# Performance work log

Measured on AMD Instinct MI355X. Metric: run time of the kernel, lower is better.

Reference implementation:

```python
import jax, jax.numpy as jnp
import numpy as np

EMBED_DIM = 32
DELTA_V = 0.5
DELTA_D = 3.0
NUM_LABELS = 20  # instance labels are 1..NUM_LABELS; 0 is background


def _safe_sqrt(x):
    # sqrt with zero-safe gradient (matches norm of identical points -> 0)
    s = jnp.where(x > 0, x, 1.0)
    return jnp.where(x > 0, jnp.sqrt(s), 0.0)


def _per_batch(emb, seg):
    # emb: [D, N], seg: [N] int labels in 0..L (0 = background)
    D, N = emb.shape
    L = NUM_LABELS
    dt = emb.dtype
    ones = jnp.ones((N,), dt)
    counts = jax.ops.segment_sum(ones, seg, num_segments=L + 1)          # [L+1]
    sums = jax.ops.segment_sum(emb.T, seg, num_segments=L + 1)          # [L+1, D]
    means = sums / jnp.maximum(counts, 1.0)[:, None]                     # [L+1, D]
    present = (counts > 0).at[0].set(False)                              # [L+1]
    num_lanes = jnp.sum(present.astype(dt))

    # --- variance (pull) loss: each pixel vs its own instance centroid ---
    mpix = means[seg]                                                    # [N, D] gather
    sq = jnp.sum((emb.T - mpix) ** 2, axis=1)                            # [N]
    d = _safe_sqrt(sq)
    v = jnp.maximum(d - DELTA_V, 0.0) ** 2 * (seg > 0).astype(dt)        # background excluded
    vsum = jax.ops.segment_sum(v, seg, num_segments=L + 1)               # [L+1]
    vmean = vsum / jnp.maximum(counts, 1.0)
    var_loss = jnp.sum(vmean * present.astype(dt)) / jnp.maximum(num_lanes, 1.0)
    var_loss = jnp.where(num_lanes > 0, var_loss, jnp.zeros((), dt))

    # --- distance (push) loss between present centroids ---
    m = means[1:]                                                        # [L, D]
    p = present[1:]                                                      # [L]
    sqd = jnp.sum((m[:, None, :] - m[None, :, :]) ** 2, axis=-1)         # [L, L]
    dist = _safe_sqrt(sqd)
    pair = (p[:, None] & p[None, :]) & ~jnp.eye(L, dtype=bool)
    dl = jnp.sum(jnp.maximum(DELTA_D - dist, 0.0) ** 2 * pair.astype(dt))
    denom = jnp.maximum(num_lanes * (num_lanes - 1.0), 1.0)
    dist_loss = jnp.where(num_lanes > 1, dl / denom / 2.0, jnp.zeros((), dt))
    return var_loss, dist_loss


def setup_inputs() -> dict:
    key = jax.random.key(0)
    k1, k2 = jax.random.split(key)
    B, D, N = 8, EMBED_DIM, 65536  # 256x256 BEV raster flattened
    embedding = jax.random.normal(k1, (B, D, N), dtype=jnp.float32)
    seg_gt = jax.random.randint(k2, (B, N), 0, NUM_LABELS + 1, dtype=jnp.int32)
    return {"embedding": embedding, "seg_gt": seg_gt}


def reference(embedding, seg_gt):
    var_b, dist_b = jax.vmap(_per_batch)(embedding, seg_gt)  # [B], [B]
    var_loss = jnp.mean(var_b)
    dist_loss = jnp.mean(dist_b)
    reg_loss = jnp.zeros((), embedding.dtype)
    return (var_loss, dist_loss, reg_loss)
```

## Files before the change

### kernel.cpp

```cpp
#include <hip/hip_runtime.h>
#include <hip/hip_cooperative_groups.h>
namespace cg = cooperative_groups;

#define NSEG 21
#define NLBL 20
#define DIM  32
#define NS   64
#define NREP 16
#define DV   0.5f
#define DD   3.0f
#define BATCH 8
#define N_PIX 65536
#define SMS  36
#define DYNB (128*512 + 1024)

using short8 = __attribute__((ext_vector_type(8))) short;
using f32x4  = __attribute__((ext_vector_type(4))) float;

#define P_OFF  0
#define C2_OFF (BATCH*DIM*NLBL*NS)
#define M_OFF  (C2_OFF + BATCH*NLBL*NS)
#define CN_OFF (M_OFF + BATCH*NLBL*DIM)
#define V_OFF  (CN_OFF + BATCH*NLBL)
#define PB_OFF (V_OFF + BATCH*NLBL*NS)

__device__ __forceinline__ short bf16rne(float f) {
  const unsigned u = __builtin_bit_cast(unsigned, f);
  return (short)((u + 0x7FFFu + ((u >> 16) & 1u)) >> 16);
}

__device__ __forceinline__ void momentsBody(const float* __restrict__ emb,
                                            const int* __restrict__ seg,
                                            float* __restrict__ ws,
                                            float* lred, ushort* tile,
                                            unsigned char* segt,
                                            int bx, int b, int tid) {
  const int wv = tid >> 6, lane = tid & 63;
  const int lr = lane & 15, lg = lane >> 4;
  const float* rowA0 = emb + ((size_t)b * DIM + lr) * N_PIX;
  const float* rowA1 = rowA0 + (size_t)16 * N_PIX;
  const int*   segb  = seg + (size_t)b * N_PIX;

  f32x4 s00 = {0,0,0,0}, s01 = {0,0,0,0}, s10 = {0,0,0,0}, s11 = {0,0,0,0};
  f32x4 c0  = {0,0,0,0}, c1  = {0,0,0,0};
  short8 ones;
  #pragma unroll
  for (int j = 0; j < 8; ++j) ones[j] = (short)0x3F80;

  #pragma unroll 2
  for (int t = 0; t < 8; ++t) {
    const int kl = wv * 256 + t * 32 + lg * 8;
    const int koff = bx * 1024 + kl;
    const float4 a00 = *(const float4*)(rowA0 + koff);
    const float4 a01 = *(const float4*)(rowA0 + koff + 4);
    const float4 a10 = *(const float4*)(rowA1 + koff);
    const float4 a11 = *(const float4*)(rowA1 + koff + 4);
    const int4   g0  = *(const int4*)(segb + koff);
    const int4   g1  = *(const int4*)(segb + koff + 4);

    short8 fa0, fa1, fb0, fb1;
    fa0[0] = bf16rne(a00.x); fa0[1] = bf16rne(a00.y);
    fa0[2] = bf16rne(a00.z); fa0[3] = bf16rne(a00.w);
    fa0[4] = bf16rne(a01.x); fa0[5] = bf16rne(a01.y);
    fa0[6] = bf16rne(a01.z); fa0[7] = bf16rne(a01.w);
    fa1[0] = bf16rne(a10.x); fa1[1] = bf16rne(a10.y);
    fa1[2] = bf16rne(a10.z); fa1[3] = bf16rne(a10.w);
    fa1[4] = bf16rne(a11.x); fa1[5] = bf16rne(a11.y);
    fa1[6] = bf16rne(a11.z); fa1[7] = bf16rne(a11.w);
    const int lab0 = lr + 1, lab1 = lr + 17;
    fb0[0] = (g0.x == lab0) ? (short)0x3F80 : (short)0;
    fb0[1] = (g0.y == lab0) ? (short)0x3F80 : (short)0;
    fb0[2] = (g0.z == lab0) ? (short)0x3F80 : (short)0;
    fb0[3] = (g0.w == lab0) ? (short)0x3F80 : (short)0;
    fb0[4] = (g1.x == lab0) ? (short)0x3F80 : (short)0;
    fb0[5] = (g1.y == lab0) ? (short)0x3F80 : (short)0;
    fb0[6] = (g1.z == lab0) ? (short)0x3F80 : (short)0;
    fb0[7] = (g1.w == lab0) ? (short)0x3F80 : (short)0;
    fb1[0] = (g0.x == lab1) ? (short)0x3F80 : (short)0;
    fb1[1] = (g0.y == lab1) ? (short)0x3F80 : (short)0;
    fb1[2] = (g0.z == lab1) ? (short)0x3F80 : (short)0;
    fb1[3] = (g0.w == lab1) ? (short)0x3F80 : (short)0;
    fb1[4] = (g1.x == lab1) ? (short)0x3F80 : (short)0;
    fb1[5] = (g1.y == lab1) ? (short)0x3F80 : (short)0;
    fb1[6] = (g1.z == lab1) ? (short)0x3F80 : (short)0;
    fb1[7] = (g1.w == lab1) ? (short)0x3F80 : (short)0;

    const int o = kl >> 3, om = o & 7;
    *(short8*)&tile[o * 256 + ((lr ^ om) << 3)] = fa0;
    *(short8*)&tile[o * 256 + (((lr ^ om) + 16) << 3)] = fa1;
    if (lr == 0) {
      unsigned long long pk =
          (unsigned long long)(g0.x & 255)        | ((unsigned long long)(g0.y & 255) << 8) |
          ((unsigned long long)(g0.z & 255) << 16) | ((unsigned long long)(g0.w & 255) << 24) |
          ((unsigned long long)(g1.x & 255) << 32) | ((unsigned long long)(g1.y & 255) << 40) |
          ((unsigned long long)(g1.z & 255) << 48) | ((unsigned long long)(g1.w & 255) << 56);
      *(unsigned long long*)&segt[o * 8] = pk;
    }

    s00 = __builtin_amdgcn_mfma_f32_16x16x32_bf16(fa0, fb0, s00, 0, 0, 0);
    s01 = __builtin_amdgcn_mfma_f32_16x16x32_bf16(fa0, fb1, s01, 0, 0, 0);
    s10 = __builtin_amdgcn_mfma_f32_16x16x32_bf16(fa1, fb0, s10, 0, 0, 0);
    s11 = __builtin_amdgcn_mfma_f32_16x16x32_bf16(fa1, fb1, s11, 0, 0, 0);
    c0  = __builtin_amdgcn_mfma_f32_16x16x32_bf16(ones, fb0, c0, 0, 0, 0);
    c1  = __builtin_amdgcn_mfma_f32_16x16x32_bf16(ones, fb1, c1, 0, 0, 0);
  }

  float vals[24];
  #pragma unroll
  for (int r = 0; r < 4; ++r) {
    vals[0 * 4 + r] = s00[r]; vals[1 * 4 + r] = s01[r];
    vals[2 * 4 + r] = s10[r]; vals[3 * 4 + r] = s11[r];
    vals[4 * 4 + r] = c0[r];  vals[5 * 4 + r] = c1[r];
  }
  #pragma unroll
  for (int w = 0; w < 4; ++w) {
    if (wv == w) {
      float* base = lred + lane * 4;
      if (w == 0) {
        #pragma unroll
        for (int f = 0; f < 6; ++f)
          #pragma unroll
          for (int r = 0; r < 4; ++r) base[f * 256 + r] = vals[f * 4 + r];
      } else {
        #pragma unroll
        for (int f = 0; f < 6; ++f)
          #pragma unroll
          for (int r = 0; r < 4; ++r) base[f * 256 + r] += vals[f * 4 + r];
      }
    }
    __syncthreads();
  }
  for (int i = tid; i < 1536; i += 256) {
    const float v = lred[i];
    const int f = i >> 8, ln = (i >> 2) & 63, r = i & 3;
    const int col = ln & 15, row = ((ln >> 4) << 2) | r;
    if (f < 4) {
      const int d = (f >> 1) * 16 + row;
      const int lcol = (f & 1) * 16 + col;
      if (lcol < NLBL)
        ws[P_OFF + (((size_t)(b * DIM + d) * NLBL) + lcol) * NS + bx] = v;
    } else {
      const int lcol = (f & 1) * 16 + col;
      if (row == 0 && lcol < NLBL)
        ws[C2_OFF + ((size_t)b * NLBL + lcol) * NS + bx] = v;
    }
  }
}

__device__ __forceinline__ void meansBody(float* __restrict__ ws, float* s_c,
                                          int bx8, int b, int tid) {
  if (tid < NLBL) {
    const float4* cp = (const float4*)(ws + C2_OFF + ((size_t)b * NLBL + tid) * NS);
    float q0 = 0.f, q1 = 0.f, q2 = 0.f, q3 = 0.f;
    #pragma unroll
    for (int k = 0; k < NS / 4; k += 4) {
      const float4 v0 = cp[k], v1 = cp[k + 1], v2 = cp[k + 2], v3 = cp[k + 3];
      q0 += v0.x + v0.y + v0.z + v0.w;
      q1 += v1.x + v1.y + v1.z + v1.w;
      q2 += v2.x + v2.y + v2.z + v2.w;
      q3 += v3.x + v3.y + v3.z + v3.w;
    }
    const float c = q0 + q1 + q2 + q3;
    if (bx8 == 0) ws[CN_OFF + b * NLBL + tid] = c;
    s_c[tid] = fmaxf(c, 1.f);
  }
  __syncthreads();
  if (tid < 80) {
    const int m = bx8 * 80 + tid;
    const int l = m >> 5, d = m & 31;
    const float4* pp = (const float4*)(ws + P_OFF + (((size_t)(b * DIM + d) * NLBL) + l) * NS);
    float q0 = 0.f, q1 = 0.f, q2 = 0.f, q3 = 0.f;
    #pragma unroll
    for (int k = 0; k < NS / 4; k += 4) {
      const float4 v0 = pp[k], v1 = pp[k + 1], v2 = pp[k + 2], v3 = pp[k + 3];
      q0 += v0.x + v0.y + v0.z + v0.w;
      q1 += v1.x + v1.y + v1.z + v1.w;
      q2 += v2.x + v2.y + v2.z + v2.w;
      q3 += v3.x + v3.y + v3.z + v3.w;
    }
    ws[M_OFF + (size_t)b * NLBL * DIM + m] = (q0 + q1 + q2 + q3) / s_c[l];
  }
}

__device__ __forceinline__ void loadMeans(const float* __restrict__ ws,
                                          float* s_m, int b, int tid) {
  for (int i = tid; i < NSEG * SMS; i += 256) s_m[i] = 0.f;
  __syncthreads();
  if (tid < 160) {
    const float4 v = ((const float4*)(ws + M_OFF + (size_t)b * NLBL * DIM))[tid];
    const int flat = tid * 4, l = flat >> 5, d = flat & 31;
    float* dst = &s_m[(l + 1) * SMS + d];
    dst[0] = v.x; dst[1] = v.y; dst[2] = v.z; dst[3] = v.w;
  }
}

__device__ __forceinline__ void finalBody(float* __restrict__ ws,
                                          float* s_m, float* s_c, float* s_vs,
                                          int* s_p, float* s_red, int b, int tid) {
  const int wv = tid >> 6, lane = tid & 63;
  if (tid < 160) {
    const int g = tid >> 3, j = tid & 7;
    const float4* v4 = (const float4*)(ws + V_OFF + ((size_t)b * NLBL + g) * NS + j * 8);
    const float4 a = v4[0], c = v4[1];
    float s = a.x + a.y + a.z + a.w + c.x + c.y + c.z + c.w;
    s += __shfl_xor(s, 1, 64); s += __shfl_xor(s, 2, 64); s += __shfl_xor(s, 4, 64);
    if (j == 0) s_vs[g] = s;
  }
  if (tid < NLBL) {
    const float c = ws[CN_OFF + b * NLBL + tid];
    s_c[tid] = c;
    s_p[tid] = (c > 0.f) ? 1 : 0;
  }
  __syncthreads();
  loadMeans(ws, s_m, b, tid);
  __syncthreads();

  float dl = 0.f;
  for (int p = tid; p < NLBL * NLBL; p += 256) {
    const int i = p / NLBL, j = p - (p / NLBL) * NLBL;
    if (i != j && s_p[i] && s_p[j]) {
      float sq = 0.f;
      #pragma unroll
      for (int d = 0; d < DIM; ++d) {
        const float t = s_m[(i + 1) * SMS + d] - s_m[(j + 1) * SMS + d];
        sq += t * t;
      }
      const float r = DD - sqrtf(sq);
      if (r > 0.f) dl += r * r;
    }
  }
  #pragma unroll
  for (int off = 32; off; off >>= 1) dl += __shfl_xor(dl, off, 64);
  if (lane == 0) s_red[wv] = dl;
  __syncthreads();
  if (tid == 0) {
    const float dsum = s_red[0] + s_red[1] + s_red[2] + s_red[3];
    float nl = 0.f, var = 0.f;
    for (int l = 0; l < NLBL; ++l)
      if (s_p[l]) { nl += 1.f; var += s_vs[l] / s_c[l]; }
    ws[PB_OFF + b * 2]     = (nl > 0.f) ? var / nl : 0.f;
    ws[PB_OFF + b * 2 + 1] = (nl > 1.f) ? dsum / fmaxf(nl * (nl - 1.f), 1.f) * 0.5f : 0.f;
  }
}

__device__ __forceinline__ void outBody(const float* __restrict__ ws,
                                        float* __restrict__ out, int tid) {
  if (tid < 64) {
    float v = 0.f, d = 0.f;
    if (tid < BATCH) {
      v = ws[PB_OFF + tid * 2];
      d = ws[PB_OFF + tid * 2 + 1];
    }
    #pragma unroll
    for (int off = 4; off; off >>= 1) { v += __shfl_xor(v, off, 64); d += __shfl_xor(d, off, 64); }
    if (tid == 0) {
      out[0] = v / (float)BATCH;
      out[1] = d / (float)BATCH;
      out[2] = 0.f;
    }
  }
}

__global__ __launch_bounds__(256, 2)
void k_fused(const float* __restrict__ emb, const int* __restrict__ seg,
             float* __restrict__ ws, float* __restrict__ out) {
  extern __shared__ __align__(16) char dynls[];
  ushort* tile = (ushort*)dynls;
  unsigned char* segt = (unsigned char*)(dynls + 65536);
  __shared__ __align__(16) float lred[1536];
  __shared__ __align__(16) float s_m[NSEG * SMS];
  __shared__ float s_v[NREP * NSEG];
  __shared__ float s_c[NLBL];
  __shared__ float s_vs[NLBL];
  __shared__ int   s_p[NLBL];
  __shared__ float s_red[4];
  cg::grid_group gg = cg::this_grid();
  const int tid = threadIdx.x, bx = blockIdx.x, b = blockIdx.y;

  momentsBody(emb, seg, ws, lred, tile, segt, bx, b, tid);
  gg.sync();
  if (bx < 8) meansBody(ws, s_c, bx, b, tid);
  gg.sync();

  for (int i = tid; i < NREP * NSEG; i += 256) s_v[i] = 0.f;
  loadMeans(ws, s_m, b, tid);
  __syncthreads();
  {
    const int px0 = tid * 4;
    const int o = px0 >> 3, om = o & 7, p8 = px0 & 7;
    const int la0 = segt[px0], la1 = segt[px0 + 1], la2 = segt[px0 + 2], la3 = segt[px0 + 3];
    float q0 = 0.f, q1 = 0.f, q2 = 0.f, q3 = 0.f;
    #pragma unroll
    for (int db = 0; db < 8; ++db) {
      const f32x4 m0 = *(const f32x4*)&s_m[la0 * SMS + db * 4];
      const f32x4 m1 = *(const f32x4*)&s_m[la1 * SMS + db * 4];
      const f32x4 m2 = *(const f32x4*)&s_m[la2 * SMS + db * 4];
      const f32x4 m3 = *(const f32x4*)&s_m[la3 * SMS + db * 4];
      #pragma unroll
      for (int dd = 0; dd < 4; ++dd) {
        const int d = db * 4 + dd;
        const ushort4 ev = *(const ushort4*)&tile[o * 256 + ((d ^ om) << 3) + p8];
        float t;
        t = __builtin_bit_cast(float, (unsigned)ev.x << 16) - m0[dd]; q0 += t * t;
        t = __builtin_bit_cast(float, (unsigned)ev.y << 16) - m1[dd]; q1 += t * t;
        t = __builtin_bit_cast(float, (unsigned)ev.z << 16) - m2[dd]; q2 += t * t;
        t = __builtin_bit_cast(float, (unsigned)ev.w << 16) - m3[dd]; q3 += t * t;
      }
    }
    const int rb = (tid & (NREP - 1)) * NSEG;
    if (la0 > 0) { const float r = sqrtf(q0) - DV; if (r > 0.f) atomicAdd(&s_v[rb + la0], r * r); }
    if (la1 > 0) { const float r = sqrtf(q1) - DV; if (r > 0.f) atomicAdd(&s_v[rb + la1], r * r); }
    if (la2 > 0) { const float r = sqrtf(q2) - DV; if (r > 0.f) atomicAdd(&s_v[rb + la2], r * r); }
    if (la3 > 0) { const float r = sqrtf(q3) - DV; if (r > 0.f) atomicAdd(&s_v[rb + la3], r * r); }
  }
  __syncthreads();
  if (tid < NLBL) {
    float v = 0.f;
    #pragma unroll
    for (int r = 0; r < NREP; ++r) v += s_v[r * NSEG + (tid + 1)];
    ws[V_OFF + ((size_t)b * NLBL + tid) * NS + bx] = v;
  }
  gg.sync();
  if (bx == 0) finalBody(ws, s_m, s_c, s_vs, s_p, s_red, b, tid);
  gg.sync();
  if (bx == 0 && b == 0) outBody(ws, out, tid);
}

__global__ __launch_bounds__(256)
void k_moments(const float* __restrict__ emb, const int* __restrict__ seg,
               float* __restrict__ ws) {
  extern __shared__ __align__(16) char dynls[];
  ushort* tile = (ushort*)dynls;
  unsigned char* segt = (unsigned char*)(dynls + 65536);
  __shared__ __align__(16) float lred[1536];
  momentsBody(emb, seg, ws, lred, tile, segt, blockIdx.x, blockIdx.y, threadIdx.x);
}
__global__ __launch_bounds__(256)
void k_means(float* __restrict__ ws) {
  __shared__ float s_c[NLBL];
  meansBody(ws, s_c, blockIdx.x, blockIdx.y, threadIdx.x);
}
__global__ __launch_bounds__(256)
void k_varG(const float* __restrict__ emb, const int* __restrict__ seg,
            float* __restrict__ ws) {
  __shared__ __align__(16) float s_m[NSEG * SMS];
  __shared__ float s_v[NREP * NSEG];
  const int tid = threadIdx.x, bx = blockIdx.x, b = blockIdx.y;
  for (int i = tid; i < NREP * NSEG; i += 256) s_v[i] = 0.f;
  loadMeans(ws, s_m, b, tid);
  __syncthreads();
  const int n0 = bx * 1024 + tid * 4;
  const int4 sl = *(const int4*)(seg + (size_t)b * N_PIX + n0);
  const float4* e4 = (const float4*)(emb + (size_t)b * DIM * N_PIX + n0);
  float q0 = 0.f, q1 = 0.f, q2 = 0.f, q3 = 0.f;
  #pragma unroll 8
  for (int d = 0; d < DIM; ++d) {
    const float4 e = e4[d * (N_PIX / 4)];
    float t;
    t = e.x - s_m[sl.x * SMS + d]; q0 += t * t;
    t = e.y - s_m[sl.y * SMS + d]; q1 += t * t;
    t = e.z - s_m[sl.z * SMS + d]; q2 += t * t;
    t = e.w - s_m[sl.w * SMS + d]; q3 += t * t;
  }
  const int rb = (tid & (NREP - 1)) * NSEG;
  if (sl.x > 0) { const float r = sqrtf(q0) - DV; if (r > 0.f) atomicAdd(&s_v[rb + sl.x], r * r); }
  if (sl.y > 0) { const float r = sqrtf(q1) - DV; if (r > 0.f) atomicAdd(&s_v[rb + sl.y], r * r); }
  if (sl.z > 0) { const float r = sqrtf(q2) - DV; if (r > 0.f) atomicAdd(&s_v[rb + sl.z], r * r); }
  if (sl.w > 0) { const float r = sqrtf(q3) - DV; if (r > 0.f) atomicAdd(&s_v[rb + sl.w], r * r); }
  __syncthreads();
  if (tid < NLBL) {
    float v = 0.f;
    #pragma unroll
    for (int r = 0; r < NREP; ++r) v += s_v[r * NSEG + (tid + 1)];
    ws[V_OFF + ((size_t)b * NLBL + tid) * NS + bx] = v;
  }
}
__global__ __launch_bounds__(256)
void k_final(float* __restrict__ ws) {
  __shared__ __align__(16) float s_m[NSEG * SMS];
  __shared__ float s_c[NLBL];
  __shared__ float s_vs[NLBL];
  __shared__ int   s_p[NLBL];
  __shared__ float s_red[4];
  finalBody(ws, s_m, s_c, s_vs, s_p, s_red, blockIdx.x, threadIdx.x);
}
__global__ __launch_bounds__(64)
void k_out(const float* __restrict__ ws, float* __restrict__ out) {
  outBody(ws, out, threadIdx.x);
}

extern "C" void kernel_launch(void* const* d_in, const int* in_sizes, int n_in,
                              void* d_out, int out_size, void* d_ws, size_t ws_size,
                              hipStream_t stream) {
  const float* emb = (const float*)d_in[0];
  const int*   seg = (const int*)d_in[1];
  float* out = (float*)d_out;
  float* ws  = (float*)d_ws;

  int maxB = 0;
  bool coop = false;
  if (hipOccupancyMaxActiveBlocksPerMultiprocessor(&maxB, (const void*)k_fused, 256, DYNB)
        == hipSuccess)
    coop = ((long)maxB * 256 >= (long)NS * BATCH);
  if (coop) {
    void* args[] = {(void*)&emb, (void*)&seg, (void*)&ws, (void*)&out};
    if (hipLaunchCooperativeKernel((const void*)k_fused, dim3(NS, BATCH), dim3(256),
                                   args, DYNB, stream) == hipSuccess)
      return;
  }
  k_moments<<<dim3(NS, BATCH), 256, DYNB, stream>>>(emb, seg, ws);
  k_means  <<<dim3(8, BATCH), 256, 0, stream>>>(ws);
  k_varG   <<<dim3(NS, BATCH), 256, 0, stream>>>(emb, seg, ws);
  k_final  <<<dim3(BATCH), 256, 0, stream>>>(ws);
  k_out    <<<1, 64, 0, stream>>>(ws, out);
}
```

Before: 43.19 us.

## Compute means redundantly per block to drop grid syncs and finalize via atomics

Every block now reduces the per-slice partial moments for its own batch into local shared-memory means, instead of a subset of blocks writing means to global memory and then passing a grid barrier. The final per-batch results are added into the output with atomics, which also removes the last two grid syncs and the separate output stage. This reduces the cooperative kernel from four grid-wide barriers to two. In exchange, every block redundantly reads about 40K floats of partial sums from L2, and the output's floating-point accumulation order is no longer deterministic.

After: 51.17 us. 1.18x slower.

```diff
diff --git a/kernel.cpp b/kernel.cpp
--- a/kernel.cpp
+++ b/kernel.cpp
@@ -19,9 +19,7 @@
 
 #define P_OFF  0
 #define C2_OFF (BATCH*DIM*NLBL*NS)
-#define M_OFF  (C2_OFF + BATCH*NLBL*NS)
-#define CN_OFF (M_OFF + BATCH*NLBL*DIM)
-#define V_OFF  (CN_OFF + BATCH*NLBL)
+#define V_OFF  (C2_OFF + BATCH*NLBL*NS)
 #define PB_OFF (V_OFF + BATCH*NLBL*NS)
 
 __device__ __forceinline__ short bf16rne(float f) {
@@ -147,56 +145,77 @@
   }
 }
 
-__device__ __forceinline__ void meansBody(float* __restrict__ ws, float* s_c,
-                                          int bx8, int b, int tid) {
-  if (tid < NLBL) {
-    const float4* cp = (const float4*)(ws + C2_OFF + ((size_t)b * NLBL + tid) * NS);
+__device__ __forceinline__ void meansLocal(const float* __restrict__ ws,
+                                           float* s_m, float* s_c, int* s_p,
+                                           int b, int tid) {
+  if (tid < 160) {
+    const int g = tid >> 3, j = tid & 7;
+    const float4* cp = (const float4*)(ws + C2_OFF + ((size_t)b * NLBL + g) * NS + j * 8);
+    const float4 a = cp[0], c4 = cp[1];
+    float c = a.x + a.y + a.z + a.w + c4.x + c4.y + c4.z + c4.w;
+    c += __shfl_xor(c, 1, 64); c += __shfl_xor(c, 2, 64); c += __shfl_xor(c, 4, 64);
+    if (j == 0) { s_c[g] = c; s_p[g] = (c > 0.f) ? 1 : 0; }
+  }
+  for (int i = tid; i < SMS; i += 256) s_m[i] = 0.f;
+  __syncthreads();
+  for (int i = tid; i < NLBL * DIM; i += 256) {
+    const int d = i / NLBL, l = i - (i / NLBL) * NLBL;
+    const float4* pp = (const float4*)(ws + P_OFF + ((size_t)b * DIM * NLBL + i) * NS);
     float q0 = 0.f, q1 = 0.f, q2 = 0.f, q3 = 0.f;
     #pragma unroll
-    for (int k = 0; k < NS / 4; k += 4) {
-      const float4 v0 = cp[k], v1 = cp[k + 1], v2 = cp[k + 2], v3 = cp[k + 3];
-      q0 += v0.x + v0.y + v0.z + v0.w;
-      q1 += v1.x + v1.y + v1.z + v1.w;
-      q2 += v2.x + v2.y + v2.z + v2.w;
-      q3 += v3.x + v3.y + v3.z + v3.w;
-    }
-    const float c = q0 + q1 + q2 + q3;
-    if (bx8 == 0) ws[CN_OFF + b * NLBL + tid] = c;
-    s_c[tid] = fmaxf(c, 1.f);
-  }
-  __syncthreads();
-  if (tid < 80) {
-    const int m = bx8 * 80 + tid;
-    const int l = m >> 5, d = m & 31;
-    const float4* pp = (const float4*)(ws + P_OFF + (((size_t)(b * DIM + d) * NLBL) + l) * NS);
-    float q0 = 0.f, q1 = 0.f, q2 = 0.f, q3 = 0.f;
-    #pragma unroll
-    for (int k = 0; k < NS / 4; k += 4) {
+    for (int k = 0; k < 16; k += 4) {
       const float4 v0 = pp[k], v1 = pp[k + 1], v2 = pp[k + 2], v3 = pp[k + 3];
       q0 += v0.x + v0.y + v0.z + v0.w;
       q1 += v1.x + v1.y + v1.z + v1.w;
       q2 += v2.x + v2.y + v2.z + v2.w;
       q3 += v3.x + v3.y + v3.z + v3.w;
     }
-    ws[M_OFF + (size_t)b * NLBL * DIM + m] = (q0 + q1 + q2 + q3) / s_c[l];
-  }
-}
-
-__device__ __forceinline__ void loadMeans(const float* __restrict__ ws,
-                                          float* s_m, int b, int tid) {
-  for (int i = tid; i < NSEG * SMS; i += 256) s_m[i] = 0.f;
-  __syncthreads();
-  if (tid < 160) {
-    const float4 v = ((const float4*)(ws + M_OFF + (size_t)b * NLBL * DIM))[tid];
-    const int flat = tid * 4, l = flat >> 5, d = flat & 31;
-    float* dst = &s_m[(l + 1) * SMS + d];
-    dst[0] = v.x; dst[1] = v.y; dst[2] = v.z; dst[3] = v.w;
-  }
-}
-
-__device__ __forceinline__ void finalBody(float* __restrict__ ws,
-                                          float* s_m, float* s_c, float* s_vs,
-                                          int* s_p, float* s_red, int b, int tid) {
+    s_m[(l + 1) * SMS + d] = (q0 + q1 + q2 + q3) / fmaxf(s_c[l], 1.f);
+  }
+}
+
+__device__ __forceinline__ void varTile(const ushort* tile, const unsigned char* segt,
+                                        const float* s_m, float* s_v,
+                                        float* __restrict__ ws, int bx, int b, int tid) {
+  const int px0 = tid * 4;
+  const int o = px0 >> 3, om = o & 7, p8 = px0 & 7;
+  const int la0 = segt[px0], la1 = segt[px0 + 1], la2 = segt[px0 + 2], la3 = segt[px0 + 3];
+  float q0 = 0.f, q1 = 0.f, q2 = 0.f, q3 = 0.f;
+  #pragma unroll
+  for (int db = 0; db < 8; ++db) {
+    const f32x4 m0 = *(const f32x4*)&s_m[la0 * SMS + db * 4];
+    const f32x4 m1 = *(const f32x4*)&s_m[la1 * SMS + db * 4];
+    const f32x4 m2 = *(const f32x4*)&s_m[la2 * SMS + db * 4];
+    const f32x4 m3 = *(const f32x4*)&s_m[la3 * SMS + db * 4];
+    #pragma unroll
+    for (int dd = 0; dd < 4; ++dd) {
+      const int d = db * 4 + dd;
+      const ushort4 ev = *(const ushort4*)&tile[o * 256 + ((d ^ om) << 3) + p8];
+      float t;
+      t = __builtin_bit_cast(float, (unsigned)ev.x << 16) - m0[dd]; q0 += t * t;
+      t = __builtin_bit_cast(float, (unsigned)ev.y << 16) - m1[dd]; q1 += t * t;
+      t = __builtin_bit_cast(float, (unsigned)ev.z << 16) - m2[dd]; q2 += t * t;
+      t = __builtin_bit_cast(float, (unsigned)ev.w << 16) - m3[dd]; q3 += t * t;
+    }
+  }
+  const int rb = (tid & (NREP - 1)) * NSEG;
+  if (la0 > 0) { const float r = sqrtf(q0) - DV; if (r > 0.f) atomicAdd(&s_v[rb + la0], r * r); }
+  if (la1 > 0) { const float r = sqrtf(q1) - DV; if (r > 0.f) atomicAdd(&s_v[rb + la1], r * r); }
+  if (la2 > 0) { const float r = sqrtf(q2) - DV; if (r > 0.f) atomicAdd(&s_v[rb + la2], r * r); }
+  if (la3 > 0) { const float r = sqrtf(q3) - DV; if (r > 0.f) atomicAdd(&s_v[rb + la3], r * r); }
+  __syncthreads();
+  if (tid < NLBL) {
+    float v = 0.f;
+    #pragma unroll
+    for (int r = 0; r < NREP; ++r) v += s_v[r * NSEG + (tid + 1)];
+    ws[V_OFF + ((size_t)b * NLBL + tid) * NS + bx] = v;
+  }
+}
+
+__device__ __forceinline__ void finalCore(const float* __restrict__ ws,
+                                          const float* s_m, const float* s_c,
+                                          const int* s_p, float* s_vs, float* s_red,
+                                          int b, int tid, float* vb, float* db_) {
   const int wv = tid >> 6, lane = tid & 63;
   if (tid < 160) {
     const int g = tid >> 3, j = tid & 7;
@@ -206,15 +225,7 @@
     s += __shfl_xor(s, 1, 64); s += __shfl_xor(s, 2, 64); s += __shfl_xor(s, 4, 64);
     if (j == 0) s_vs[g] = s;
   }
-  if (tid < NLBL) {
-    const float c = ws[CN_OFF + b * NLBL + tid];
-    s_c[tid] = c;
-    s_p[tid] = (c > 0.f) ? 1 : 0;
-  }
-  __syncthreads();
-  loadMeans(ws, s_m, b, tid);
-  __syncthreads();
-
+  __syncthreads();
   float dl = 0.f;
   for (int p = tid; p < NLBL * NLBL; p += 256) {
     const int i = p / NLBL, j = p - (p / NLBL) * NLBL;
@@ -238,26 +249,8 @@
     float nl = 0.f, var = 0.f;
     for (int l = 0; l < NLBL; ++l)
       if (s_p[l]) { nl += 1.f; var += s_vs[l] / s_c[l]; }
-    ws[PB_OFF + b * 2]     = (nl > 0.f) ? var / nl : 0.f;
-    ws[PB_OFF + b * 2 + 1] = (nl > 1.f) ? dsum / fmaxf(nl * (nl - 1.f), 1.f) * 0.5f : 0.f;
-  }
-}
-
-__device__ __forceinline__ void outBody(const float* __restrict__ ws,
-                                        float* __restrict__ out, int tid) {
-  if (tid < 64) {
-    float v = 0.f, d = 0.f;
-    if (tid < BATCH) {
-      v = ws[PB_OFF + tid * 2];
-      d = ws[PB_OFF + tid * 2 + 1];
-    }
-    #pragma unroll
-    for (int off = 4; off; off >>= 1) { v += __shfl_xor(v, off, 64); d += __shfl_xor(d, off, 64); }
-    if (tid == 0) {
-      out[0] = v / (float)BATCH;
-      out[1] = d / (float)BATCH;
-      out[2] = 0.f;
-    }
+    *vb  = (nl > 0.f) ? var / nl : 0.f;
+    *db_ = (nl > 1.f) ? dsum / fmaxf(nl * (nl - 1.f), 1.f) * 0.5f : 0.f;
   }
 }
 
@@ -278,52 +271,23 @@
   const int tid = threadIdx.x, bx = blockIdx.x, b = blockIdx.y;
 
   momentsBody(emb, seg, ws, lred, tile, segt, bx, b, tid);
+  if (bx == 0 && b == 0 && tid < 3) out[tid] = 0.f;
   gg.sync();
-  if (bx < 8) meansBody(ws, s_c, bx, b, tid);
+
+  for (int i = tid; i < NREP * NSEG; i += 256) s_v[i] = 0.f;
+  meansLocal(ws, s_m, s_c, s_p, b, tid);
+  __syncthreads();
+  varTile(tile, segt, s_m, s_v, ws, bx, b, tid);
   gg.sync();
 
-  for (int i = tid; i < NREP * NSEG; i += 256) s_v[i] = 0.f;
-  loadMeans(ws, s_m, b, tid);
-  __syncthreads();
-  {
-    const int px0 = tid * 4;
-    const int o = px0 >> 3, om = o & 7, p8 = px0 & 7;
-    const int la0 = segt[px0], la1 = segt[px0 + 1], la2 = segt[px0 + 2], la3 = segt[px0 + 3];
-    float q0 = 0.f, q1 = 0.f, q2 = 0.f, q3 = 0.f;
-    #pragma unroll
-    for (int db = 0; db < 8; ++db) {
-      const f32x4 m0 = *(const f32x4*)&s_m[la0 * SMS + db * 4];
-      const f32x4 m1 = *(const f32x4*)&s_m[la1 * SMS + db * 4];
-      const f32x4 m2 = *(const f32x4*)&s_m[la2 * SMS + db * 4];
-      const f32x4 m3 = *(const f32x4*)&s_m[la3 * SMS + db * 4];
-      #pragma unroll
-      for (int dd = 0; dd < 4; ++dd) {
-        const int d = db * 4 + dd;
-        const ushort4 ev = *(const ushort4*)&tile[o * 256 + ((d ^ om) << 3) + p8];
-        float t;
-        t = __builtin_bit_cast(float, (unsigned)ev.x << 16) - m0[dd]; q0 += t * t;
-        t = __builtin_bit_cast(float, (unsigned)ev.y << 16) - m1[dd]; q1 += t * t;
-        t = __builtin_bit_cast(float, (unsigned)ev.z << 16) - m2[dd]; q2 += t * t;
-        t = __builtin_bit_cast(float, (unsigned)ev.w << 16) - m3[dd]; q3 += t * t;
-      }
-    }
-    const int rb = (tid & (NREP - 1)) * NSEG;
-    if (la0 > 0) { const float r = sqrtf(q0) - DV; if (r > 0.f) atomicAdd(&s_v[rb + la0], r * r); }
-    if (la1 > 0) { const float r = sqrtf(q1) - DV; if (r > 0.f) atomicAdd(&s_v[rb + la1], r * r); }
-    if (la2 > 0) { const float r = sqrtf(q2) - DV; if (r > 0.f) atomicAdd(&s_v[rb + la2], r * r); }
-    if (la3 > 0) { const float r = sqrtf(q3) - DV; if (r > 0.f) atomicAdd(&s_v[rb + la3], r * r); }
-  }
-  __syncthreads();
-  if (tid < NLBL) {
-    float v = 0.f;
-    #pragma unroll
-    for (int r = 0; r < NREP; ++r) v += s_v[r * NSEG + (tid + 1)];
-    ws[V_OFF + ((size_t)b * NLBL + tid) * NS + bx] = v;
-  }
-  gg.sync();
-  if (bx == 0) finalBody(ws, s_m, s_c, s_vs, s_p, s_red, b, tid);
-  gg.sync();
-  if (bx == 0 && b == 0) outBody(ws, out, tid);
+  if (bx == 0) {
+    float vb, db_;
+    finalCore(ws, s_m, s_c, s_p, s_vs, s_red, b, tid, &vb, &db_);
+    if (tid == 0) {
+      atomicAdd(&out[0], vb * (1.f / BATCH));
+      atomicAdd(&out[1], db_ * (1.f / BATCH));
+    }
+  }
 }
 
 __global__ __launch_bounds__(256)
@@ -336,18 +300,15 @@
   momentsBody(emb, seg, ws, lred, tile, segt, blockIdx.x, blockIdx.y, threadIdx.x);
 }
 __global__ __launch_bounds__(256)
-void k_means(float* __restrict__ ws) {
-  __shared__ float s_c[NLBL];
-  meansBody(ws, s_c, blockIdx.x, blockIdx.y, threadIdx.x);
-}
-__global__ __launch_bounds__(256)
 void k_varG(const float* __restrict__ emb, const int* __restrict__ seg,
             float* __restrict__ ws) {
   __shared__ __align__(16) float s_m[NSEG * SMS];
   __shared__ float s_v[NREP * NSEG];
+  __shared__ float s_c[NLBL];
+  __shared__ int   s_p[NLBL];
   const int tid = threadIdx.x, bx = blockIdx.x, b = blockIdx.y;
   for (int i = tid; i < NREP * NSEG; i += 256) s_v[i] = 0.f;
-  loadMeans(ws, s_m, b, tid);
+  meansLocal(ws, s_m, s_c, s_p, b, tid);
   __syncthreads();
   const int n0 = bx * 1024 + tid * 4;
   const int4 sl = *(const int4*)(seg + (size_t)b * N_PIX + n0);
@@ -382,11 +343,31 @@
   __shared__ float s_vs[NLBL];
   __shared__ int   s_p[NLBL];
   __shared__ float s_red[4];
-  finalBody(ws, s_m, s_c, s_vs, s_p, s_red, blockIdx.x, threadIdx.x);
+  const int b = blockIdx.x, tid = threadIdx.x;
+  meansLocal(ws, s_m, s_c, s_p, b, tid);
+  __syncthreads();
+  float vb, db_;
+  finalCore(ws, s_m, s_c, s_p, s_vs, s_red, b, tid, &vb, &db_);
+  if (tid == 0) {
+    ws[PB_OFF + b * 2]     = vb;
+    ws[PB_OFF + b * 2 + 1] = db_;
+  }
 }
 __global__ __launch_bounds__(64)
 void k_out(const float* __restrict__ ws, float* __restrict__ out) {
-  outBody(ws, out, threadIdx.x);
+  const int tid = threadIdx.x;
+  float v = 0.f, d = 0.f;
+  if (tid < BATCH) {
+    v = ws[PB_OFF + tid * 2];
+    d = ws[PB_OFF + tid * 2 + 1];
+  }
+  #pragma unroll
+  for (int off = 4; off; off >>= 1) { v += __shfl_xor(v, off, 64); d += __shfl_xor(d, off, 64); }
+  if (tid == 0) {
+    out[0] = v / (float)BATCH;
+    out[1] = d / (float)BATCH;
+    out[2] = 0.f;
+  }
 }
 
 extern "C" void kernel_launch(void* const* d_in, const int* in_sizes, int n_in,
@@ -409,7 +390,6 @@
       return;
   }
   k_moments<<<dim3(NS, BATCH), 256, DYNB, stream>>>(emb, seg, ws);
-  k_means  <<<dim3(8, BATCH), 256, 0, stream>>>(ws);
   k_varG   <<<dim3(NS, BATCH), 256, 0, stream>>>(emb, seg, ws);
   k_final  <<<dim3(BATCH), 256, 0, stream>>>(ws);
   k_out    <<<1, 64, 0, stream>>>(ws, out);
```

## Double grid to 128 blocks per batch, shrink LDS, and drop the final grid sync

Applied to the files above, without the earlier changes.

Halves the pixels each block handles (512 instead of 1024) and doubles the blocks per batch to 128. Shared memory shrinks by unioning lred with s_m and s_v, which allows 4 blocks per CU so the cooperative grid of 1024 blocks fits. The last grid barrier and the separate output pass are replaced by atomic accumulation into out, which is zeroed before the first barrier. The cost is more partial-sum slots to reduce in the final stage, more blocks taking part in each grid sync, and atomic ordering making the result non-deterministic.

Result: slower. 46.18 us (+6.9%).

```diff
diff --git a/kernel.cpp b/kernel.cpp
--- a/kernel.cpp
+++ b/kernel.cpp
@@ -5,14 +5,17 @@
 #define NSEG 21
 #define NLBL 20
 #define DIM  32
-#define NS   64
+#define NS   128
 #define NREP 16
 #define DV   0.5f
 #define DD   3.0f
 #define BATCH 8
 #define N_PIX 65536
 #define SMS  36
-#define DYNB (128*512 + 1024)
+#define TILE_B 32768
+#define SEGT_B 512
+#define UNI_B  6144
+#define DYNB   (TILE_B + SEGT_B + UNI_B)
 
 using short8 = __attribute__((ext_vector_type(8))) short;
 using f32x4  = __attribute__((ext_vector_type(4))) float;
@@ -48,9 +51,9 @@
   for (int j = 0; j < 8; ++j) ones[j] = (short)0x3F80;
 
   #pragma unroll 2
-  for (int t = 0; t < 8; ++t) {
-    const int kl = wv * 256 + t * 32 + lg * 8;
-    const int koff = bx * 1024 + kl;
+  for (int t = 0; t < 4; ++t) {
+    const int kl = wv * 32 + t * 128 + lg * 8;
+    const int koff = bx * 512 + kl;
     const float4 a00 = *(const float4*)(rowA0 + koff);
     const float4 a01 = *(const float4*)(rowA0 + koff + 4);
     const float4 a10 = *(const float4*)(rowA1 + koff);
@@ -194,15 +197,49 @@
   }
 }
 
-__device__ __forceinline__ void finalBody(float* __restrict__ ws,
-                                          float* s_m, float* s_c, float* s_vs,
-                                          int* s_p, float* s_red, int b, int tid) {
+__device__ __forceinline__ void varTile(const ushort* tile, const unsigned char* segt,
+                                        const float* s_m, float* s_v,
+                                        float* __restrict__ ws, int bx, int b, int tid) {
+  const int px0 = tid * 2;
+  const int o = px0 >> 3, om = o & 7, p8 = px0 & 7;
+  const int la0 = segt[px0], la1 = segt[px0 + 1];
+  float q0 = 0.f, q1 = 0.f;
+  #pragma unroll
+  for (int db = 0; db < 8; ++db) {
+    const f32x4 m0 = *(const f32x4*)&s_m[la0 * SMS + db * 4];
+    const f32x4 m1 = *(const f32x4*)&s_m[la1 * SMS + db * 4];
+    #pragma unroll
+    for (int dd = 0; dd < 4; ++dd) {
+      const int d = db * 4 + dd;
+      const ushort2 ev = *(const ushort2*)&tile[o * 256 + ((d ^ om) << 3) + p8];
+      float t;
+      t = __builtin_bit_cast(float, (unsigned)ev.x << 16) - m0[dd]; q0 += t * t;
+      t = __builtin_bit_cast(float, (unsigned)ev.y << 16) - m1[dd]; q1 += t * t;
+    }
+  }
+  const int rb = (tid & (NREP - 1)) * NSEG;
+  if (la0 > 0) { const float r = sqrtf(q0) - DV; if (r > 0.f) atomicAdd(&s_v[rb + la0], r * r); }
+  if (la1 > 0) { const float r = sqrtf(q1) - DV; if (r > 0.f) atomicAdd(&s_v[rb + la1], r * r); }
+  __syncthreads();
+  if (tid < NLBL) {
+    float v = 0.f;
+    #pragma unroll
+    for (int r = 0; r < NREP; ++r) v += s_v[r * NSEG + (tid + 1)];
+    ws[V_OFF + ((size_t)b * NLBL + tid) * NS + bx] = v;
+  }
+}
+
+__device__ __forceinline__ void finalCore(const float* __restrict__ ws,
+                                          const float* s_m, float* s_c, float* s_vs,
+                                          int* s_p, float* s_red,
+                                          int b, int tid, float* vb, float* db_) {
   const int wv = tid >> 6, lane = tid & 63;
   if (tid < 160) {
     const int g = tid >> 3, j = tid & 7;
-    const float4* v4 = (const float4*)(ws + V_OFF + ((size_t)b * NLBL + g) * NS + j * 8);
-    const float4 a = v4[0], c = v4[1];
-    float s = a.x + a.y + a.z + a.w + c.x + c.y + c.z + c.w;
+    const float4* v4 = (const float4*)(ws + V_OFF + ((size_t)b * NLBL + g) * NS + j * 16);
+    float s = 0.f;
+    #pragma unroll
+    for (int k = 0; k < 4; ++k) { const float4 v = v4[k]; s += v.x + v.y + v.z + v.w; }
     s += __shfl_xor(s, 1, 64); s += __shfl_xor(s, 2, 64); s += __shfl_xor(s, 4, 64);
     if (j == 0) s_vs[g] = s;
   }
@@ -212,9 +249,6 @@
     s_p[tid] = (c > 0.f) ? 1 : 0;
   }
   __syncthreads();
-  loadMeans(ws, s_m, b, tid);
-  __syncthreads();
-
   float dl = 0.f;
   for (int p = tid; p < NLBL * NLBL; p += 256) {
     const int i = p / NLBL, j = p - (p / NLBL) * NLBL;
@@ -238,38 +272,21 @@
     float nl = 0.f, var = 0.f;
     for (int l = 0; l < NLBL; ++l)
       if (s_p[l]) { nl += 1.f; var += s_vs[l] / s_c[l]; }
-    ws[PB_OFF + b * 2]     = (nl > 0.f) ? var / nl : 0.f;
-    ws[PB_OFF + b * 2 + 1] = (nl > 1.f) ? dsum / fmaxf(nl * (nl - 1.f), 1.f) * 0.5f : 0.f;
-  }
-}
-
-__device__ __forceinline__ void outBody(const float* __restrict__ ws,
-                                        float* __restrict__ out, int tid) {
-  if (tid < 64) {
-    float v = 0.f, d = 0.f;
-    if (tid < BATCH) {
-      v = ws[PB_OFF + tid * 2];
-      d = ws[PB_OFF + tid * 2 + 1];
-    }
-    #pragma unroll
-    for (int off = 4; off; off >>= 1) { v += __shfl_xor(v, off, 64); d += __shfl_xor(d, off, 64); }
-    if (tid == 0) {
-      out[0] = v / (float)BATCH;
-      out[1] = d / (float)BATCH;
-      out[2] = 0.f;
-    }
-  }
-}
-
-__global__ __launch_bounds__(256, 2)
+    *vb  = (nl > 0.f) ? var / nl : 0.f;
+    *db_ = (nl > 1.f) ? dsum / fmaxf(nl * (nl - 1.f), 1.f) * 0.5f : 0.f;
+  }
+}
+
+__global__ __launch_bounds__(256, 4)
 void k_fused(const float* __restrict__ emb, const int* __restrict__ seg,
              float* __restrict__ ws, float* __restrict__ out) {
   extern __shared__ __align__(16) char dynls[];
   ushort* tile = (ushort*)dynls;
-  unsigned char* segt = (unsigned char*)(dynls + 65536);
-  __shared__ __align__(16) float lred[1536];
-  __shared__ __align__(16) float s_m[NSEG * SMS];
-  __shared__ float s_v[NREP * NSEG];
+  unsigned char* segt = (unsigned char*)(dynls + TILE_B);
+  float* uni = (float*)(dynls + TILE_B + SEGT_B);
+  float* lred = uni;
+  float* s_m  = uni;
+  float* s_v  = uni + NSEG * SMS;
   __shared__ float s_c[NLBL];
   __shared__ float s_vs[NLBL];
   __shared__ int   s_p[NLBL];
@@ -278,52 +295,26 @@
   const int tid = threadIdx.x, bx = blockIdx.x, b = blockIdx.y;
 
   momentsBody(emb, seg, ws, lred, tile, segt, bx, b, tid);
+  if (bx == 0 && b == 0 && tid < 3) out[tid] = 0.f;
   gg.sync();
+
   if (bx < 8) meansBody(ws, s_c, bx, b, tid);
   gg.sync();
 
   for (int i = tid; i < NREP * NSEG; i += 256) s_v[i] = 0.f;
   loadMeans(ws, s_m, b, tid);
   __syncthreads();
-  {
-    const int px0 = tid * 4;
-    const int o = px0 >> 3, om = o & 7, p8 = px0 & 7;
-    const int la0 = segt[px0], la1 = segt[px0 + 1], la2 = segt[px0 + 2], la3 = segt[px0 + 3];
-    float q0 = 0.f, q1 = 0.f, q2 = 0.f, q3 = 0.f;
-    #pragma unroll
-    for (int db = 0; db < 8; ++db) {
-      const f32x4 m0 = *(const f32x4*)&s_m[la0 * SMS + db * 4];
-      const f32x4 m1 = *(const f32x4*)&s_m[la1 * SMS + db * 4];
-      const f32x4 m2 = *(const f32x4*)&s_m[la2 * SMS + db * 4];
-      const f32x4 m3 = *(const f32x4*)&s_m[la3 * SMS + db * 4];
-      #pragma unroll
-      for (int dd = 0; dd < 4; ++dd) {
-        const int d = db * 4 + dd;
-        const ushort4 ev = *(const ushort4*)&tile[o * 256 + ((d ^ om) << 3) + p8];
-        float t;
-        t = __builtin_bit_cast(float, (unsigned)ev.x << 16) - m0[dd]; q0 += t * t;
-        t = __builtin_bit_cast(float, (unsigned)ev.y << 16) - m1[dd]; q1 += t * t;
-        t = __builtin_bit_cast(float, (unsigned)ev.z << 16) - m2[dd]; q2 += t * t;
-        t = __builtin_bit_cast(float, (unsigned)ev.w << 16) - m3[dd]; q3 += t * t;
-      }
-    }
-    const int rb = (tid & (NREP - 1)) * NSEG;
-    if (la0 > 0) { const float r = sqrtf(q0) - DV; if (r > 0.f) atomicAdd(&s_v[rb + la0], r * r); }
-    if (la1 > 0) { const float r = sqrtf(q1) - DV; if (r > 0.f) atomicAdd(&s_v[rb + la1], r * r); }
-    if (la2 > 0) { const float r = sqrtf(q2) - DV; if (r > 0.f) atomicAdd(&s_v[rb + la2], r * r); }
-    if (la3 > 0) { const float r = sqrtf(q3) - DV; if (r > 0.f) atomicAdd(&s_v[rb + la3], r * r); }
-  }
-  __syncthreads();
-  if (tid < NLBL) {
-    float v = 0.f;
-    #pragma unroll
-    for (int r = 0; r < NREP; ++r) v += s_v[r * NSEG + (tid + 1)];
-    ws[V_OFF + ((size_t)b * NLBL + tid) * NS + bx] = v;
-  }
+  varTile(tile, segt, s_m, s_v, ws, bx, b, tid);
   gg.sync();
-  if (bx == 0) finalBody(ws, s_m, s_c, s_vs, s_p, s_red, b, tid);
-  gg.sync();
-  if (bx == 0 && b == 0) outBody(ws, out, tid);
+
+  if (bx == 0) {
+    float vb, db_;
+    finalCore(ws, s_m, s_c, s_vs, s_p, s_red, b, tid, &vb, &db_);
+    if (tid == 0) {
+      atomicAdd(&out[0], vb * (1.f / BATCH));
+      atomicAdd(&out[1], db_ * (1.f / BATCH));
+    }
+  }
 }
 
 __global__ __launch_bounds__(256)
@@ -331,8 +322,8 @@
                float* __restrict__ ws) {
   extern __shared__ __align__(16) char dynls[];
   ushort* tile = (ushort*)dynls;
-  unsigned char* segt = (unsigned char*)(dynls + 65536);
-  __shared__ __align__(16) float lred[1536];
+  unsigned char* segt = (unsigned char*)(dynls + TILE_B);
+  float* lred = (float*)(dynls + TILE_B + SEGT_B);
   momentsBody(emb, seg, ws, lred, tile, segt, blockIdx.x, blockIdx.y, threadIdx.x);
 }
 __global__ __launch_bounds__(256)
@@ -349,24 +340,21 @@
   for (int i = tid; i < NREP * NSEG; i += 256) s_v[i] = 0.f;
   loadMeans(ws, s_m, b, tid);
   __syncthreads();
-  const int n0 = bx * 1024 + tid * 4;
-  const int4 sl = *(const int4*)(seg + (size_t)b * N_PIX + n0);
-  const float4* e4 = (const float4*)(emb + (size_t)b * DIM * N_PIX + n0);
-  float q0 = 0.f, q1 = 0.f, q2 = 0.f, q3 = 0.f;
+  const int n0 = bx * 512;
+  const int2 sl = ((const int2*)(seg + (size_t)b * N_PIX + n0))[tid];
+  const float2* e2 = (const float2*)(emb + (size_t)b * DIM * N_PIX + n0) + tid;
+  const int mx = sl.x * SMS, my = sl.y * SMS;
+  float q0 = 0.f, q1 = 0.f;
   #pragma unroll 8
   for (int d = 0; d < DIM; ++d) {
-    const float4 e = e4[d * (N_PIX / 4)];
+    const float2 e = e2[d * (N_PIX / 2)];
     float t;
-    t = e.x - s_m[sl.x * SMS + d]; q0 += t * t;
-    t = e.y - s_m[sl.y * SMS + d]; q1 += t * t;
-    t = e.z - s_m[sl.z * SMS + d]; q2 += t * t;
-    t = e.w - s_m[sl.w * SMS + d]; q3 += t * t;
+    t = e.x - s_m[mx + d]; q0 += t * t;
+    t = e.y - s_m[my + d]; q1 += t * t;
   }
   const int rb = (tid & (NREP - 1)) * NSEG;
   if (sl.x > 0) { const float r = sqrtf(q0) - DV; if (r > 0.f) atomicAdd(&s_v[rb + sl.x], r * r); }
   if (sl.y > 0) { const float r = sqrtf(q1) - DV; if (r > 0.f) atomicAdd(&s_v[rb + sl.y], r * r); }
-  if (sl.z > 0) { const float r = sqrtf(q2) - DV; if (r > 0.f) atomicAdd(&s_v[rb + sl.z], r * r); }
-  if (sl.w > 0) { const float r = sqrtf(q3) - DV; if (r > 0.f) atomicAdd(&s_v[rb + sl.w], r * r); }
   __syncthreads();
   if (tid < NLBL) {
     float v = 0.f;
@@ -382,11 +370,31 @@
   __shared__ float s_vs[NLBL];
   __shared__ int   s_p[NLBL];
   __shared__ float s_red[4];
-  finalBody(ws, s_m, s_c, s_vs, s_p, s_red, blockIdx.x, threadIdx.x);
+  const int b = blockIdx.x, tid = threadIdx.x;
+  loadMeans(ws, s_m, b, tid);
+  __syncthreads();
+  float vb, db_;
+  finalCore(ws, s_m, s_c, s_vs, s_p, s_red, b, tid, &vb, &db_);
+  if (tid == 0) {
+    ws[PB_OFF + b * 2]     = vb;
+    ws[PB_OFF + b * 2 + 1] = db_;
+  }
 }
 __global__ __launch_bounds__(64)
 void k_out(const float* __restrict__ ws, float* __restrict__ out) {
-  outBody(ws, out, threadIdx.x);
+  const int tid = threadIdx.x;
+  float v = 0.f, d = 0.f;
+  if (tid < BATCH) {
+    v = ws[PB_OFF + tid * 2];
+    d = ws[PB_OFF + tid * 2 + 1];
+  }
+  #pragma unroll
+  for (int off = 4; off; off >>= 1) { v += __shfl_xor(v, off, 64); d += __shfl_xor(d, off, 64); }
+  if (tid == 0) {
+    out[0] = v / (float)BATCH;
+    out[1] = d / (float)BATCH;
+    out[2] = 0.f;
+  }
 }
 
 extern "C" void kernel_launch(void* const* d_in, const int* in_sizes, int n_in,
```
